# Kernel optimization log

Hardware: AMD Instinct MI355X
Metric: run time of the kernel (lower is better)

Reference implementation:

```python
import jax, jax.numpy as jnp
import numpy as np

EMBED_DIM = 1024
NUM_HEADS = 16
HEAD_DIM = EMBED_DIM // NUM_HEADS


def setup_inputs() -> dict:
    key = jax.random.key(0)
    ks = jax.random.split(key, 5)
    x = jax.random.normal(ks[0], (2, 2048, EMBED_DIM), dtype=jnp.float32)
    s_in = 1.0 / np.sqrt(EMBED_DIM)
    W_qkv = jax.random.uniform(ks[1], (EMBED_DIM, 3 * EMBED_DIM), minval=-s_in, maxval=s_in, dtype=jnp.float32)
    b_qkv = jax.random.uniform(ks[2], (3 * EMBED_DIM,), minval=-s_in, maxval=s_in, dtype=jnp.float32)
    W_out = jax.random.uniform(ks[3], (EMBED_DIM, EMBED_DIM), minval=-s_in, maxval=s_in, dtype=jnp.float32)
    b_out = jax.random.uniform(ks[4], (EMBED_DIM,), minval=-s_in, maxval=s_in, dtype=jnp.float32)
    return {"x": x, "W_qkv": W_qkv, "b_qkv": b_qkv, "W_out": W_out, "b_out": b_out}


def reference(x, W_qkv, b_qkv, W_out, b_out):
    B, S, D = x.shape
    H, Dh = NUM_HEADS, HEAD_DIM
    qkv = x @ W_qkv + b_qkv                       # [B, S, 3D]
    q, k, v = jnp.split(qkv, 3, axis=-1)
    # [B, S, D] -> [B, H, S, Dh]
    q = q.reshape(B, S, H, Dh).transpose(0, 2, 1, 3)
    k = k.reshape(B, S, H, Dh).transpose(0, 2, 1, 3)
    v = v.reshape(B, S, H, Dh).transpose(0, 2, 1, 3)
    scores = jnp.einsum('bhqd,bhkd->bhqk', q, k) / jnp.sqrt(jnp.float32(Dh))
    probs = jax.nn.softmax(scores, axis=-1)       # [B, H, S, S]
    attn = jnp.einsum('bhqk,bhkd->bhqd', probs, v)
    attn = attn.transpose(0, 2, 1, 3).reshape(B, S, D)
    return attn @ W_out + b_out
```

## Files before the change

### kernel.cpp

```cpp
#include <hip/hip_runtime.h>
#include <hip/hip_bf16.h>

#define DEV __device__ __forceinline__

typedef __bf16 bf16x8 __attribute__((ext_vector_type(8)));
typedef float f32x4 __attribute__((ext_vector_type(4)));
typedef float f32x16 __attribute__((ext_vector_type(16)));
using u16 = unsigned short;
using u32 = unsigned int;

static constexpr int S = 2048;
static constexpr int D = 1024;
static constexpr float SCQ = 0.125f * 1.44269504088896340736f;

DEV u16 f2bf(float f) {
  unsigned u = __builtin_bit_cast(unsigned, f);
  u += 0x7fffu + ((u >> 16) & 1u);
  return (u16)(u >> 16);
}
DEV u16 f2bfr(float f) {
  return (u16)((__builtin_bit_cast(u32, f) + 0x8000u) >> 16);
}
DEV u32 pk2(float a, float b) {
  u32 ua = __builtin_bit_cast(u32, a) + 0x8000u;
  u32 ub = __builtin_bit_cast(u32, b) + 0x8000u;
  return __builtin_amdgcn_perm(ub, ua, 0x07060302);
}

__global__ __launch_bounds__(256) void k_prep(const float* __restrict__ x, u16* __restrict__ Xb,
                                              const float* __restrict__ Wqkv, u16* __restrict__ WqkvT,
                                              const float* __restrict__ Wout, u16* __restrict__ WoutT) {
  __shared__ float t[32][33];
  const int bid = blockIdx.x;
  const int tid = threadIdx.x;
  if (bid < 4096) {
    const int i = bid * 256 + tid;
    const float4 v = reinterpret_cast<const float4*>(x)[i];
    ushort4 o;
    o.x = f2bf(v.x); o.y = f2bf(v.y); o.z = f2bf(v.z); o.w = f2bf(v.w);
    reinterpret_cast<ushort4*>(Xb)[i] = o;
    return;
  }
  const float* in;
  u16* out;
  int R, C, bx, by;
  if (bid < 4096 + 3072) {
    const int b = bid - 4096;
    in = Wqkv; out = WqkvT; R = 1024; C = 3072;
    bx = b % 96; by = b / 96;
  } else {
    const int b = bid - 7168;
    in = Wout; out = WoutT; R = 1024; C = 1024;
    bx = b & 31; by = b >> 5;
  }
  const int tx = tid & 31, ty = tid >> 5;
  const int c0 = bx * 32, r0 = by * 32;
  for (int i = ty; i < 32; i += 8)
    t[i][tx] = in[(size_t)(r0 + i) * C + c0 + tx];
  __syncthreads();
  for (int i = ty; i < 32; i += 8)
    out[(size_t)(c0 + i) * R + r0 + tx] = f2bf(t[tx][i]);
}

template <int MODE, int TN>
__global__ __launch_bounds__(256) void k_gemm(const u16* __restrict__ A, const u16* __restrict__ Bt,
                                              const float* __restrict__ bias, int M, int N, int K,
                                              u16* __restrict__ Qb, u16* __restrict__ Kb,
                                              u16* __restrict__ Vt, float* __restrict__ outF) {
  constexpr int NJ = TN / 32;
  __shared__ u16 As[128][40];
  __shared__ u16 Bs[TN][40];
  const int tid = threadIdx.x;
  const int lane = tid & 63, wave = tid >> 6;
  const int l15 = lane & 15, quad = lane >> 4;
  const int m0 = blockIdx.y * 128, n0 = blockIdx.x * TN;
  const int wm = (wave >> 1) * 64, wn = (wave & 1) * (TN / 2);
  const int row0 = tid >> 2, c0 = (tid & 3) * 8;
  const int row1 = row0 + 64;

  f32x4 acc[4][NJ];
#pragma unroll
  for (int i = 0; i < 4; i++)
#pragma unroll
    for (int j = 0; j < NJ; j++) acc[i][j] = (f32x4){0.f, 0.f, 0.f, 0.f};

  uint4 pa0 = *reinterpret_cast<const uint4*>(&A[(size_t)(m0 + row0) * K + c0]);
  uint4 pa1 = *reinterpret_cast<const uint4*>(&A[(size_t)(m0 + row1) * K + c0]);
  uint4 pb0 = *reinterpret_cast<const uint4*>(&Bt[(size_t)(n0 + row0) * K + c0]);
  uint4 pb1;
  if constexpr (TN == 128) pb1 = *reinterpret_cast<const uint4*>(&Bt[(size_t)(n0 + row1) * K + c0]);

  for (int kk = 0; kk < K; kk += 32) {
    __syncthreads();
    *reinterpret_cast<uint4*>(&As[row0][c0]) = pa0;
    *reinterpret_cast<uint4*>(&As[row1][c0]) = pa1;
    *reinterpret_cast<uint4*>(&Bs[row0 & (TN - 1)][c0]) = pb0;
    if constexpr (TN == 128) *reinterpret_cast<uint4*>(&Bs[row1][c0]) = pb1;
    __syncthreads();
    if (kk + 32 < K) {
      pa0 = *reinterpret_cast<const uint4*>(&A[(size_t)(m0 + row0) * K + kk + 32 + c0]);
      pa1 = *reinterpret_cast<const uint4*>(&A[(size_t)(m0 + row1) * K + kk + 32 + c0]);
      pb0 = *reinterpret_cast<const uint4*>(&Bt[(size_t)(n0 + row0) * K + kk + 32 + c0]);
      if constexpr (TN == 128)
        pb1 = *reinterpret_cast<const uint4*>(&Bt[(size_t)(n0 + row1) * K + kk + 32 + c0]);
    }
    bf16x8 af[4], bfv[NJ];
#pragma unroll
    for (int i = 0; i < 4; i++)
      af[i] = *reinterpret_cast<const bf16x8*>(&As[wm + i * 16 + l15][quad * 8]);
#pragma unroll
    for (int j = 0; j < NJ; j++)
      bfv[j] = *reinterpret_cast<const bf16x8*>(&Bs[wn + j * 16 + l15][quad * 8]);
#pragma unroll
    for (int i = 0; i < 4; i++)
#pragma unroll
      for (int j = 0; j < NJ; j++)
        acc[i][j] = __builtin_amdgcn_mfma_f32_16x16x32_bf16(af[i], bfv[j], acc[i][j], 0, 0, 0);
  }

  if constexpr (MODE == 0) {
    __shared__ u16 LT[64][136];
    if (n0 >= 2048) {
      const int b = m0 >> 11, sbase = m0 & 2047;
#pragma unroll
      for (int p = 0; p < 2; p++) {
        __syncthreads();
        if ((wave & 1) == p) {
#pragma unroll
          for (int j = 0; j < NJ; j++) {
            const int n = n0 + wn + j * 16 + l15;
            const float vb = bias[n];
#pragma unroll
            for (int i = 0; i < 4; i++) {
              uint2 pw;
              pw.x = pk2(acc[i][j][0] + vb, acc[i][j][1] + vb);
              pw.y = pk2(acc[i][j][2] + vb, acc[i][j][3] + vb);
              *reinterpret_cast<uint2*>(&LT[j * 16 + l15][wm + i * 16 + quad * 4]) = pw;
            }
          }
        }
        __syncthreads();
        const int h = ((n0 - 2048) >> 6) + p;
        const int bh = b * 16 + h;
        const int nl = tid >> 2, cc = (tid & 3) * 32;
        u16* dst = &Vt[((size_t)bh * 64 + nl) * S + sbase + cc];
#pragma unroll
        for (int k = 0; k < 4; k++)
          reinterpret_cast<uint4*>(dst)[k] = *reinterpret_cast<const uint4*>(&LT[nl][cc + k * 8]);
      }
    } else {
#pragma unroll
      for (int i = 0; i < 4; i++) {
#pragma unroll
        for (int j = 0; j < NJ; j++) {
#pragma unroll
          for (int r = 0; r < 4; r++) {
            const int m = m0 + wm + i * 16 + quad * 4 + r;
            const int n = n0 + wn + j * 16 + l15;
            const float v = acc[i][j][r] + bias[n];
            const int h = (n >> 6) & 15, dh = n & 63;
            const int b = m >> 11, s = m & 2047;
            const int bh = b * 16 + h;
            if (n < 1024) Qb[((size_t)bh * S + s) * 64 + dh] = f2bfr(v * SCQ);
            else          Kb[((size_t)bh * S + s) * 64 + dh] = f2bfr(v);
          }
        }
      }
    }
  } else {
#pragma unroll
    for (int i = 0; i < 4; i++)
#pragma unroll
      for (int j = 0; j < NJ; j++)
#pragma unroll
        for (int r = 0; r < 4; r++) {
          const int m = m0 + wm + i * 16 + quad * 4 + r;
          const int n = n0 + wn + j * 16 + l15;
          outF[(size_t)m * N + n] = acc[i][j][r] + bias[n];
        }
  }
}

__global__ __launch_bounds__(256, 2) void k_attn(const u16* __restrict__ Qb,
                                                 const u16* __restrict__ Kb,
                                                 const u16* __restrict__ Vt,
                                                 u16* __restrict__ attnB) {
  __shared__ u16 Ks[64][72];
  __shared__ u16 Vs[64][72];
  __shared__ u16 Pl[4][32][72];
  const int bh = blockIdx.y;
  const int q0 = blockIdx.x * 128;
  const int tid = threadIdx.x;
  const int lane = tid & 63, wave = tid >> 6;
  const int l31 = lane & 31, hi = lane >> 5;
  const u16* Qh = Qb + (size_t)bh * S * 64;
  const u16* Kh = Kb + (size_t)bh * S * 64;
  const u16* Vh = Vt + (size_t)bh * 64 * S;
  const int qrow = q0 + wave * 32 + l31;
  bf16x8 qf[4];
#pragma unroll
  for (int f = 0; f < 4; f++)
    qf[f] = *reinterpret_cast<const bf16x8*>(&Qh[(size_t)qrow * 64 + f * 16 + hi * 8]);

  const int r0 = tid >> 3, c0 = (tid & 7) * 8;

  float li = 0.f;
  f32x16 o0, o1;
#pragma unroll
  for (int r = 0; r < 16; r++) { o0[r] = 0.f; o1[r] = 0.f; }

  uint4 pk0 = *reinterpret_cast<const uint4*>(&Kh[(size_t)r0 * 64 + c0]);
  uint4 pk1 = *reinterpret_cast<const uint4*>(&Kh[(size_t)(r0 + 32) * 64 + c0]);
  uint4 pv0 = *reinterpret_cast<const uint4*>(&Vh[(size_t)r0 * S + c0]);
  uint4 pv1 = *reinterpret_cast<const uint4*>(&Vh[(size_t)(r0 + 32) * S + c0]);

  for (int kb = 0; kb < S / 64; kb++) {
    __syncthreads();
    *reinterpret_cast<uint4*>(&Ks[r0][c0]) = pk0;
    *reinterpret_cast<uint4*>(&Ks[r0 + 32][c0]) = pk1;
    *reinterpret_cast<uint4*>(&Vs[r0][c0]) = pv0;
    *reinterpret_cast<uint4*>(&Vs[r0 + 32][c0]) = pv1;
    __syncthreads();
    if (kb + 1 < S / 64) {
      const u16* Kn = Kh + (size_t)(kb + 1) * 64 * 64;
      pk0 = *reinterpret_cast<const uint4*>(&Kn[(size_t)r0 * 64 + c0]);
      pk1 = *reinterpret_cast<const uint4*>(&Kn[(size_t)(r0 + 32) * 64 + c0]);
      pv0 = *reinterpret_cast<const uint4*>(&Vh[(size_t)r0 * S + (kb + 1) * 64 + c0]);
      pv1 = *reinterpret_cast<const uint4*>(&Vh[(size_t)(r0 + 32) * S + (kb + 1) * 64 + c0]);
    }
    f32x16 z[2];
#pragma unroll
    for (int kt = 0; kt < 2; kt++) {
#pragma unroll
      for (int r = 0; r < 16; r++) z[kt][r] = 0.f;
#pragma unroll
      for (int f = 0; f < 4; f++) {
        const bf16x8 a = *reinterpret_cast<const bf16x8*>(&Ks[kt * 32 + l31][f * 16 + hi * 8]);
        z[kt] = __builtin_amdgcn_mfma_f32_32x32x16_bf16(a, qf[f], z[kt], 0, 0, 0);
      }
    }
    float s0 = 0.f, s1 = 0.f, s2 = 0.f, s3 = 0.f;
#pragma unroll
    for (int kt = 0; kt < 2; kt++)
#pragma unroll
      for (int r = 0; r < 16; r++) {
        const float p = __builtin_amdgcn_exp2f(z[kt][r]);
        z[kt][r] = p;
        if ((r & 3) == 0) s0 += p; else if ((r & 3) == 1) s1 += p;
        else if ((r & 3) == 2) s2 += p; else s3 += p;
      }
    li += (s0 + s1) + (s2 + s3);
#pragma unroll
    for (int kt = 0; kt < 2; kt++)
#pragma unroll
      for (int g = 0; g < 4; g++) {
        uint2 pw;
        pw.x = pk2(z[kt][g * 4 + 0], z[kt][g * 4 + 1]);
        pw.y = pk2(z[kt][g * 4 + 2], z[kt][g * 4 + 3]);
        *reinterpret_cast<uint2*>(&Pl[wave][l31][kt * 32 + g * 8 + hi * 4]) = pw;
      }
#pragma unroll
    for (int f = 0; f < 4; f++) {
      const bf16x8 bp = *reinterpret_cast<const bf16x8*>(&Pl[wave][l31][f * 16 + hi * 8]);
      const bf16x8 av0 = *reinterpret_cast<const bf16x8*>(&Vs[l31][f * 16 + hi * 8]);
      const bf16x8 av1 = *reinterpret_cast<const bf16x8*>(&Vs[32 + l31][f * 16 + hi * 8]);
      o0 = __builtin_amdgcn_mfma_f32_32x32x16_bf16(av0, bp, o0, 0, 0, 0);
      o1 = __builtin_amdgcn_mfma_f32_32x32x16_bf16(av1, bp, o1, 0, 0, 0);
    }
  }
  li += __shfl_xor(li, 32);
  const float inv = 1.f / li;
#pragma unroll
  for (int dt = 0; dt < 2; dt++) {
    const f32x16& od = dt ? o1 : o0;
#pragma unroll
    for (int g = 0; g < 4; g++) {
      uint2 ow;
      ow.x = pk2(od[g * 4 + 0] * inv, od[g * 4 + 1] * inv);
      ow.y = pk2(od[g * 4 + 2] * inv, od[g * 4 + 3] * inv);
      *reinterpret_cast<uint2*>(&Pl[wave][l31][dt * 32 + g * 8 + hi * 4]) = ow;
    }
  }
  const int b = bh >> 4, h = bh & 15;
  const int mbase = b * S + q0 + wave * 32;
  const int qr = lane >> 1, ch = (lane & 1) * 32;
  u16* dst = &attnB[(size_t)(mbase + qr) * D + h * 64 + ch];
#pragma unroll
  for (int c = 0; c < 4; c++)
    reinterpret_cast<uint4*>(dst)[c] = *reinterpret_cast<const uint4*>(&Pl[wave][qr][ch + c * 8]);
}

extern "C" void kernel_launch(void* const* d_in, const int* in_sizes, int n_in,
                              void* d_out, int out_size, void* d_ws, size_t ws_size,
                              hipStream_t stream) {
  const float* x = (const float*)d_in[0];
  const float* Wqkv = (const float*)d_in[1];
  const float* bqkv = (const float*)d_in[2];
  const float* Wout = (const float*)d_in[3];
  const float* bout = (const float*)d_in[4];
  float* out = (float*)d_out;

  char* p = (char*)d_ws;
  u16* Xb = (u16*)p;    p += (size_t)4096 * 1024 * 2;
  u16* WqkvT = (u16*)p; p += (size_t)3072 * 1024 * 2;
  u16* WoutT = (u16*)p; p += (size_t)1024 * 1024 * 2;
  u16* Qb = (u16*)p;    p += (size_t)32 * 2048 * 64 * 2;
  u16* Kb = (u16*)p;    p += (size_t)32 * 2048 * 64 * 2;
  u16* Vt = (u16*)p;    p += (size_t)32 * 64 * 2048 * 2;
  u16* attnB = (u16*)p; p += (size_t)4096 * 1024 * 2;

  k_prep<<<4096 + 3072 + 1024, 256, 0, stream>>>(x, Xb, Wqkv, WqkvT, Wout, WoutT);
  k_gemm<0, 128><<<dim3(3072 / 128, 4096 / 128), 256, 0, stream>>>(
      Xb, WqkvT, bqkv, 4096, 3072, 1024, Qb, Kb, Vt, nullptr);
  k_attn<<<dim3(2048 / 128, 32), 256, 0, stream>>>(Qb, Kb, Vt, attnB);
  k_gemm<1, 64><<<dim3(1024 / 64, 4096 / 128), 256, 0, stream>>>(
      attnB, WoutT, bout, 4096, 1024, 1024, nullptr, nullptr, nullptr, out);
}
```

Before: 200.6 us.

## Split attention over two key halves and merge partials in a combine kernel

```diff
diff --git a/kernel.cpp b/kernel.cpp
--- a/kernel.cpp
+++ b/kernel.cpp
@@ -181,14 +181,16 @@
   }
 }
 
-__global__ __launch_bounds__(256, 2) void k_attn(const u16* __restrict__ Qb,
+__global__ __launch_bounds__(256, 4) void k_attn(const u16* __restrict__ Qb,
                                                  const u16* __restrict__ Kb,
                                                  const u16* __restrict__ Vt,
-                                                 u16* __restrict__ attnB) {
+                                                 u16* __restrict__ Op0, u16* __restrict__ Op1,
+                                                 float* __restrict__ Li) {
   __shared__ u16 Ks[64][72];
   __shared__ u16 Vs[64][72];
   __shared__ u16 Pl[4][32][72];
-  const int bh = blockIdx.y;
+  const int bh = blockIdx.z;
+  const int ks = blockIdx.y;
   const int q0 = blockIdx.x * 128;
   const int tid = threadIdx.x;
   const int lane = tid & 63, wave = tid >> 6;
@@ -203,25 +205,26 @@
     qf[f] = *reinterpret_cast<const bf16x8*>(&Qh[(size_t)qrow * 64 + f * 16 + hi * 8]);
 
   const int r0 = tid >> 3, c0 = (tid & 7) * 8;
+  const int kb0 = ks * 16, kb1 = kb0 + 16;
 
   float li = 0.f;
   f32x16 o0, o1;
 #pragma unroll
   for (int r = 0; r < 16; r++) { o0[r] = 0.f; o1[r] = 0.f; }
 
-  uint4 pk0 = *reinterpret_cast<const uint4*>(&Kh[(size_t)r0 * 64 + c0]);
-  uint4 pk1 = *reinterpret_cast<const uint4*>(&Kh[(size_t)(r0 + 32) * 64 + c0]);
-  uint4 pv0 = *reinterpret_cast<const uint4*>(&Vh[(size_t)r0 * S + c0]);
-  uint4 pv1 = *reinterpret_cast<const uint4*>(&Vh[(size_t)(r0 + 32) * S + c0]);
-
-  for (int kb = 0; kb < S / 64; kb++) {
+  uint4 pk0 = *reinterpret_cast<const uint4*>(&Kh[(size_t)(kb0 * 64 + r0) * 64 + c0]);
+  uint4 pk1 = *reinterpret_cast<const uint4*>(&Kh[(size_t)(kb0 * 64 + r0 + 32) * 64 + c0]);
+  uint4 pv0 = *reinterpret_cast<const uint4*>(&Vh[(size_t)r0 * S + kb0 * 64 + c0]);
+  uint4 pv1 = *reinterpret_cast<const uint4*>(&Vh[(size_t)(r0 + 32) * S + kb0 * 64 + c0]);
+
+  for (int kb = kb0; kb < kb1; kb++) {
     __syncthreads();
     *reinterpret_cast<uint4*>(&Ks[r0][c0]) = pk0;
     *reinterpret_cast<uint4*>(&Ks[r0 + 32][c0]) = pk1;
     *reinterpret_cast<uint4*>(&Vs[r0][c0]) = pv0;
     *reinterpret_cast<uint4*>(&Vs[r0 + 32][c0]) = pv1;
     __syncthreads();
-    if (kb + 1 < S / 64) {
+    if (kb + 1 < kb1) {
       const u16* Kn = Kh + (size_t)(kb + 1) * 64 * 64;
       pk0 = *reinterpret_cast<const uint4*>(&Kn[(size_t)r0 * 64 + c0]);
       pk1 = *reinterpret_cast<const uint4*>(&Kn[(size_t)(r0 + 32) * 64 + c0]);
@@ -269,25 +272,50 @@
     }
   }
   li += __shfl_xor(li, 32);
-  const float inv = 1.f / li;
+  if (hi == 0) Li[((size_t)ks * 32 + bh) * 2048 + qrow] = li;
 #pragma unroll
   for (int dt = 0; dt < 2; dt++) {
     const f32x16& od = dt ? o1 : o0;
 #pragma unroll
     for (int g = 0; g < 4; g++) {
       uint2 ow;
-      ow.x = pk2(od[g * 4 + 0] * inv, od[g * 4 + 1] * inv);
-      ow.y = pk2(od[g * 4 + 2] * inv, od[g * 4 + 3] * inv);
+      ow.x = pk2(od[g * 4 + 0], od[g * 4 + 1]);
+      ow.y = pk2(od[g * 4 + 2], od[g * 4 + 3]);
       *reinterpret_cast<uint2*>(&Pl[wave][l31][dt * 32 + g * 8 + hi * 4]) = ow;
     }
   }
   const int b = bh >> 4, h = bh & 15;
   const int mbase = b * S + q0 + wave * 32;
   const int qr = lane >> 1, ch = (lane & 1) * 32;
-  u16* dst = &attnB[(size_t)(mbase + qr) * D + h * 64 + ch];
+  u16* Opx = ks ? Op1 : Op0;
+  u16* dst = &Opx[(size_t)(mbase + qr) * D + h * 64 + ch];
 #pragma unroll
   for (int c = 0; c < 4; c++)
     reinterpret_cast<uint4*>(dst)[c] = *reinterpret_cast<const uint4*>(&Pl[wave][qr][ch + c * 8]);
+}
+
+__global__ __launch_bounds__(256) void k_combine(const u16* __restrict__ Op0,
+                                                 const u16* __restrict__ Op1,
+                                                 const float* __restrict__ Li,
+                                                 u16* __restrict__ attnB) {
+  const int i = blockIdx.x * 256 + threadIdx.x;
+  const int e = i * 4;
+  const int m = e >> 10, n = e & 1023;
+  const int b = m >> 11, s = m & 2047, h = n >> 6;
+  const int li_idx = ((b << 4) + h) * 2048 + s;
+  const float inv = 1.f / (Li[li_idx] + Li[65536 + li_idx]);
+  const uint2 a = reinterpret_cast<const uint2*>(Op0)[i];
+  const uint2 c = reinterpret_cast<const uint2*>(Op1)[i];
+  const float v0 = __builtin_bit_cast(float, a.x << 16) + __builtin_bit_cast(float, c.x << 16);
+  const float v1 = __builtin_bit_cast(float, a.x & 0xffff0000u) +
+                   __builtin_bit_cast(float, c.x & 0xffff0000u);
+  const float v2 = __builtin_bit_cast(float, a.y << 16) + __builtin_bit_cast(float, c.y << 16);
+  const float v3 = __builtin_bit_cast(float, a.y & 0xffff0000u) +
+                   __builtin_bit_cast(float, c.y & 0xffff0000u);
+  uint2 o;
+  o.x = pk2(v0 * inv, v1 * inv);
+  o.y = pk2(v2 * inv, v3 * inv);
+  reinterpret_cast<uint2*>(attnB)[i] = o;
 }
 
 extern "C" void kernel_launch(void* const* d_in, const int* in_sizes, int n_in,
@@ -308,11 +336,15 @@
   u16* Kb = (u16*)p;    p += (size_t)32 * 2048 * 64 * 2;
   u16* Vt = (u16*)p;    p += (size_t)32 * 64 * 2048 * 2;
   u16* attnB = (u16*)p; p += (size_t)4096 * 1024 * 2;
+  u16* Op1 = (u16*)p;   p += (size_t)4096 * 1024 * 2;
+  float* Li = (float*)p; p += (size_t)2 * 32 * 2048 * 4;
+  u16* Op0 = Xb;
 
   k_prep<<<4096 + 3072 + 1024, 256, 0, stream>>>(x, Xb, Wqkv, WqkvT, Wout, WoutT);
   k_gemm<0, 128><<<dim3(3072 / 128, 4096 / 128), 256, 0, stream>>>(
       Xb, WqkvT, bqkv, 4096, 3072, 1024, Qb, Kb, Vt, nullptr);
-  k_attn<<<dim3(2048 / 128, 32), 256, 0, stream>>>(Qb, Kb, Vt, attnB);
+  k_attn<<<dim3(16, 2, 32), 256, 0, stream>>>(Qb, Kb, Vt, Op0, Op1, Li);
+  k_combine<<<4096, 256, 0, stream>>>(Op0, Op1, Li, attnB);
   k_gemm<1, 64><<<dim3(1024 / 64, 4096 / 128), 256, 0, stream>>>(
       attnB, WoutT, bout, 4096, 1024, 1024, nullptr, nullptr, nullptr, out);
 }
```

Result: slower. 205.3 us (+2.3%).

## Double GEMM K-tile to 64, alias epilogue LDS buffer, add occupancy hint

Applied to the files above, without the earlier changes.

```diff
diff --git a/kernel.cpp b/kernel.cpp
--- a/kernel.cpp
+++ b/kernel.cpp
@@ -63,20 +63,22 @@
 }
 
 template <int MODE, int TN>
-__global__ __launch_bounds__(256) void k_gemm(const u16* __restrict__ A, const u16* __restrict__ Bt,
-                                              const float* __restrict__ bias, int M, int N, int K,
-                                              u16* __restrict__ Qb, u16* __restrict__ Kb,
-                                              u16* __restrict__ Vt, float* __restrict__ outF) {
+__global__ __launch_bounds__(256, 3) void k_gemm(const u16* __restrict__ A, const u16* __restrict__ Bt,
+                                                 const float* __restrict__ bias, int M, int N, int K,
+                                                 u16* __restrict__ Qb, u16* __restrict__ Kb,
+                                                 u16* __restrict__ Vt, float* __restrict__ outF) {
   constexpr int NJ = TN / 32;
-  __shared__ u16 As[128][40];
-  __shared__ u16 Bs[TN][40];
+  constexpr int NB = (TN == 128) ? 4 : 2;
+  __shared__ u16 As[128][72];
+  __shared__ u16 Bs[TN][72];
   const int tid = threadIdx.x;
   const int lane = tid & 63, wave = tid >> 6;
   const int l15 = lane & 15, quad = lane >> 4;
   const int m0 = blockIdx.y * 128, n0 = blockIdx.x * TN;
   const int wm = (wave >> 1) * 64, wn = (wave & 1) * (TN / 2);
-  const int row0 = tid >> 2, c0 = (tid & 3) * 8;
-  const int row1 = row0 + 64;
+  const int arow = tid >> 1, acol = (tid & 1) * 32;
+  const int brow = (TN == 128) ? (tid >> 1) : (tid >> 2);
+  const int bcol = (TN == 128) ? ((tid & 1) * 32) : ((tid & 3) * 16);
 
   f32x4 acc[4][NJ];
 #pragma unroll
@@ -84,42 +86,50 @@
 #pragma unroll
     for (int j = 0; j < NJ; j++) acc[i][j] = (f32x4){0.f, 0.f, 0.f, 0.f};
 
-  uint4 pa0 = *reinterpret_cast<const uint4*>(&A[(size_t)(m0 + row0) * K + c0]);
-  uint4 pa1 = *reinterpret_cast<const uint4*>(&A[(size_t)(m0 + row1) * K + c0]);
-  uint4 pb0 = *reinterpret_cast<const uint4*>(&Bt[(size_t)(n0 + row0) * K + c0]);
-  uint4 pb1;
-  if constexpr (TN == 128) pb1 = *reinterpret_cast<const uint4*>(&Bt[(size_t)(n0 + row1) * K + c0]);
-
-  for (int kk = 0; kk < K; kk += 32) {
+  uint4 pa[4], pb[NB];
+#pragma unroll
+  for (int u = 0; u < 4; u++)
+    pa[u] = *reinterpret_cast<const uint4*>(&A[(size_t)(m0 + arow) * K + acol + u * 8]);
+#pragma unroll
+  for (int u = 0; u < NB; u++)
+    pb[u] = *reinterpret_cast<const uint4*>(&Bt[(size_t)(n0 + brow) * K + bcol + u * 8]);
+
+  for (int kk = 0; kk < K; kk += 64) {
     __syncthreads();
-    *reinterpret_cast<uint4*>(&As[row0][c0]) = pa0;
-    *reinterpret_cast<uint4*>(&As[row1][c0]) = pa1;
-    *reinterpret_cast<uint4*>(&Bs[row0 & (TN - 1)][c0]) = pb0;
-    if constexpr (TN == 128) *reinterpret_cast<uint4*>(&Bs[row1][c0]) = pb1;
+#pragma unroll
+    for (int u = 0; u < 4; u++)
+      *reinterpret_cast<uint4*>(&As[arow][acol + u * 8]) = pa[u];
+#pragma unroll
+    for (int u = 0; u < NB; u++)
+      *reinterpret_cast<uint4*>(&Bs[brow][bcol + u * 8]) = pb[u];
     __syncthreads();
-    if (kk + 32 < K) {
-      pa0 = *reinterpret_cast<const uint4*>(&A[(size_t)(m0 + row0) * K + kk + 32 + c0]);
-      pa1 = *reinterpret_cast<const uint4*>(&A[(size_t)(m0 + row1) * K + kk + 32 + c0]);
-      pb0 = *reinterpret_cast<const uint4*>(&Bt[(size_t)(n0 + row0) * K + kk + 32 + c0]);
-      if constexpr (TN == 128)
-        pb1 = *reinterpret_cast<const uint4*>(&Bt[(size_t)(n0 + row1) * K + kk + 32 + c0]);
-    }
-    bf16x8 af[4], bfv[NJ];
-#pragma unroll
-    for (int i = 0; i < 4; i++)
-      af[i] = *reinterpret_cast<const bf16x8*>(&As[wm + i * 16 + l15][quad * 8]);
-#pragma unroll
-    for (int j = 0; j < NJ; j++)
-      bfv[j] = *reinterpret_cast<const bf16x8*>(&Bs[wn + j * 16 + l15][quad * 8]);
-#pragma unroll
-    for (int i = 0; i < 4; i++)
+    if (kk + 64 < K) {
+#pragma unroll
+      for (int u = 0; u < 4; u++)
+        pa[u] = *reinterpret_cast<const uint4*>(&A[(size_t)(m0 + arow) * K + kk + 64 + acol + u * 8]);
+#pragma unroll
+      for (int u = 0; u < NB; u++)
+        pb[u] = *reinterpret_cast<const uint4*>(&Bt[(size_t)(n0 + brow) * K + kk + 64 + bcol + u * 8]);
+    }
+#pragma unroll
+    for (int h = 0; h < 2; h++) {
+      bf16x8 af[4], bfv[NJ];
+#pragma unroll
+      for (int i = 0; i < 4; i++)
+        af[i] = *reinterpret_cast<const bf16x8*>(&As[wm + i * 16 + l15][h * 32 + quad * 8]);
 #pragma unroll
       for (int j = 0; j < NJ; j++)
-        acc[i][j] = __builtin_amdgcn_mfma_f32_16x16x32_bf16(af[i], bfv[j], acc[i][j], 0, 0, 0);
+        bfv[j] = *reinterpret_cast<const bf16x8*>(&Bs[wn + j * 16 + l15][h * 32 + quad * 8]);
+#pragma unroll
+      for (int i = 0; i < 4; i++)
+#pragma unroll
+        for (int j = 0; j < NJ; j++)
+          acc[i][j] = __builtin_amdgcn_mfma_f32_16x16x32_bf16(af[i], bfv[j], acc[i][j], 0, 0, 0);
+    }
   }
 
   if constexpr (MODE == 0) {
-    __shared__ u16 LT[64][136];
+    u16(*LT)[136] = reinterpret_cast<u16(*)[136]>(&As[0][0]);
     if (n0 >= 2048) {
       const int b = m0 >> 11, sbase = m0 & 2047;
 #pragma unroll
```

Measured after the change: 311.2 us. 1.55x slower.

## Fuse x bf16 conversion into QKV GEMM and halve attention block size

Applied to the files above, without the earlier changes.

```diff
diff --git a/kernel.cpp b/kernel.cpp
--- a/kernel.cpp
+++ b/kernel.cpp
@@ -27,29 +27,19 @@
   return __builtin_amdgcn_perm(ub, ua, 0x07060302);
 }
 
-__global__ __launch_bounds__(256) void k_prep(const float* __restrict__ x, u16* __restrict__ Xb,
-                                              const float* __restrict__ Wqkv, u16* __restrict__ WqkvT,
+__global__ __launch_bounds__(256) void k_prep(const float* __restrict__ Wqkv, u16* __restrict__ WqkvT,
                                               const float* __restrict__ Wout, u16* __restrict__ WoutT) {
   __shared__ float t[32][33];
   const int bid = blockIdx.x;
   const int tid = threadIdx.x;
-  if (bid < 4096) {
-    const int i = bid * 256 + tid;
-    const float4 v = reinterpret_cast<const float4*>(x)[i];
-    ushort4 o;
-    o.x = f2bf(v.x); o.y = f2bf(v.y); o.z = f2bf(v.z); o.w = f2bf(v.w);
-    reinterpret_cast<ushort4*>(Xb)[i] = o;
-    return;
-  }
   const float* in;
   u16* out;
   int R, C, bx, by;
-  if (bid < 4096 + 3072) {
-    const int b = bid - 4096;
+  if (bid < 3072) {
     in = Wqkv; out = WqkvT; R = 1024; C = 3072;
-    bx = b % 96; by = b / 96;
+    bx = bid % 96; by = bid / 96;
   } else {
-    const int b = bid - 7168;
+    const int b = bid - 3072;
     in = Wout; out = WoutT; R = 1024; C = 1024;
     bx = b & 31; by = b >> 5;
   }
@@ -63,7 +53,7 @@
 }
 
 template <int MODE, int TN>
-__global__ __launch_bounds__(256) void k_gemm(const u16* __restrict__ A, const u16* __restrict__ Bt,
+__global__ __launch_bounds__(256) void k_gemm(const void* __restrict__ Ap, const u16* __restrict__ Bt,
                                               const float* __restrict__ bias, int M, int N, int K,
                                               u16* __restrict__ Qb, u16* __restrict__ Kb,
                                               u16* __restrict__ Vt, float* __restrict__ outF) {
@@ -77,6 +67,8 @@
   const int wm = (wave >> 1) * 64, wn = (wave & 1) * (TN / 2);
   const int row0 = tid >> 2, c0 = (tid & 3) * 8;
   const int row1 = row0 + 64;
+  const float* Af = (const float*)Ap;
+  const u16* Ab = (const u16*)Ap;
 
   f32x4 acc[4][NJ];
 #pragma unroll
@@ -84,22 +76,48 @@
 #pragma unroll
     for (int j = 0; j < NJ; j++) acc[i][j] = (f32x4){0.f, 0.f, 0.f, 0.f};
 
-  uint4 pa0 = *reinterpret_cast<const uint4*>(&A[(size_t)(m0 + row0) * K + c0]);
-  uint4 pa1 = *reinterpret_cast<const uint4*>(&A[(size_t)(m0 + row1) * K + c0]);
-  uint4 pb0 = *reinterpret_cast<const uint4*>(&Bt[(size_t)(n0 + row0) * K + c0]);
-  uint4 pb1;
+  float4 qa0, qa1, qa2, qa3;
+  uint4 pa0, pa1;
+  uint4 pb0, pb1;
+  if constexpr (MODE == 0) {
+    qa0 = *reinterpret_cast<const float4*>(&Af[(size_t)(m0 + row0) * K + c0]);
+    qa1 = *reinterpret_cast<const float4*>(&Af[(size_t)(m0 + row0) * K + c0 + 4]);
+    qa2 = *reinterpret_cast<const float4*>(&Af[(size_t)(m0 + row1) * K + c0]);
+    qa3 = *reinterpret_cast<const float4*>(&Af[(size_t)(m0 + row1) * K + c0 + 4]);
+  } else {
+    pa0 = *reinterpret_cast<const uint4*>(&Ab[(size_t)(m0 + row0) * K + c0]);
+    pa1 = *reinterpret_cast<const uint4*>(&Ab[(size_t)(m0 + row1) * K + c0]);
+  }
+  pb0 = *reinterpret_cast<const uint4*>(&Bt[(size_t)(n0 + row0) * K + c0]);
   if constexpr (TN == 128) pb1 = *reinterpret_cast<const uint4*>(&Bt[(size_t)(n0 + row1) * K + c0]);
 
   for (int kk = 0; kk < K; kk += 32) {
     __syncthreads();
-    *reinterpret_cast<uint4*>(&As[row0][c0]) = pa0;
-    *reinterpret_cast<uint4*>(&As[row1][c0]) = pa1;
+    if constexpr (MODE == 0) {
+      uint4 wa0, wa1;
+      wa0.x = pk2(qa0.x, qa0.y); wa0.y = pk2(qa0.z, qa0.w);
+      wa0.z = pk2(qa1.x, qa1.y); wa0.w = pk2(qa1.z, qa1.w);
+      wa1.x = pk2(qa2.x, qa2.y); wa1.y = pk2(qa2.z, qa2.w);
+      wa1.z = pk2(qa3.x, qa3.y); wa1.w = pk2(qa3.z, qa3.w);
+      *reinterpret_cast<uint4*>(&As[row0][c0]) = wa0;
+      *reinterpret_cast<uint4*>(&As[row1][c0]) = wa1;
+    } else {
+      *reinterpret_cast<uint4*>(&As[row0][c0]) = pa0;
+      *reinterpret_cast<uint4*>(&As[row1][c0]) = pa1;
+    }
     *reinterpret_cast<uint4*>(&Bs[row0 & (TN - 1)][c0]) = pb0;
     if constexpr (TN == 128) *reinterpret_cast<uint4*>(&Bs[row1][c0]) = pb1;
     __syncthreads();
     if (kk + 32 < K) {
-      pa0 = *reinterpret_cast<const uint4*>(&A[(size_t)(m0 + row0) * K + kk + 32 + c0]);
-      pa1 = *reinterpret_cast<const uint4*>(&A[(size_t)(m0 + row1) * K + kk + 32 + c0]);
+      if constexpr (MODE == 0) {
+        qa0 = *reinterpret_cast<const float4*>(&Af[(size_t)(m0 + row0) * K + kk + 32 + c0]);
+        qa1 = *reinterpret_cast<const float4*>(&Af[(size_t)(m0 + row0) * K + kk + 32 + c0 + 4]);
+        qa2 = *reinterpret_cast<const float4*>(&Af[(size_t)(m0 + row1) * K + kk + 32 + c0]);
+        qa3 = *reinterpret_cast<const float4*>(&Af[(size_t)(m0 + row1) * K + kk + 32 + c0 + 4]);
+      } else {
+        pa0 = *reinterpret_cast<const uint4*>(&Ab[(size_t)(m0 + row0) * K + kk + 32 + c0]);
+        pa1 = *reinterpret_cast<const uint4*>(&Ab[(size_t)(m0 + row1) * K + kk + 32 + c0]);
+      }
       pb0 = *reinterpret_cast<const uint4*>(&Bt[(size_t)(n0 + row0) * K + kk + 32 + c0]);
       if constexpr (TN == 128)
         pb1 = *reinterpret_cast<const uint4*>(&Bt[(size_t)(n0 + row1) * K + kk + 32 + c0]);
@@ -181,15 +199,15 @@
   }
 }
 
-__global__ __launch_bounds__(256, 2) void k_attn(const u16* __restrict__ Qb,
-                                                 const u16* __restrict__ Kb,
-                                                 const u16* __restrict__ Vt,
-                                                 u16* __restrict__ attnB) {
+__global__ __launch_bounds__(128) void k_attn(const u16* __restrict__ Qb,
+                                              const u16* __restrict__ Kb,
+                                              const u16* __restrict__ Vt,
+                                              u16* __restrict__ attnB) {
   __shared__ u16 Ks[64][72];
   __shared__ u16 Vs[64][72];
-  __shared__ u16 Pl[4][32][72];
+  __shared__ u16 Pl[2][32][72];
   const int bh = blockIdx.y;
-  const int q0 = blockIdx.x * 128;
+  const int q0 = blockIdx.x * 64;
   const int tid = threadIdx.x;
   const int lane = tid & 63, wave = tid >> 6;
   const int l31 = lane & 31, hi = lane >> 5;
@@ -209,24 +227,28 @@
 #pragma unroll
   for (int r = 0; r < 16; r++) { o0[r] = 0.f; o1[r] = 0.f; }
 
-  uint4 pk0 = *reinterpret_cast<const uint4*>(&Kh[(size_t)r0 * 64 + c0]);
-  uint4 pk1 = *reinterpret_cast<const uint4*>(&Kh[(size_t)(r0 + 32) * 64 + c0]);
-  uint4 pv0 = *reinterpret_cast<const uint4*>(&Vh[(size_t)r0 * S + c0]);
-  uint4 pv1 = *reinterpret_cast<const uint4*>(&Vh[(size_t)(r0 + 32) * S + c0]);
+  uint4 pk[4], pv[4];
+#pragma unroll
+  for (int u = 0; u < 4; u++) {
+    pk[u] = *reinterpret_cast<const uint4*>(&Kh[(size_t)(r0 + 16 * u) * 64 + c0]);
+    pv[u] = *reinterpret_cast<const uint4*>(&Vh[(size_t)(r0 + 16 * u) * S + c0]);
+  }
 
   for (int kb = 0; kb < S / 64; kb++) {
     __syncthreads();
-    *reinterpret_cast<uint4*>(&Ks[r0][c0]) = pk0;
-    *reinterpret_cast<uint4*>(&Ks[r0 + 32][c0]) = pk1;
-    *reinterpret_cast<uint4*>(&Vs[r0][c0]) = pv0;
-    *reinterpret_cast<uint4*>(&Vs[r0 + 32][c0]) = pv1;
+#pragma unroll
+    for (int u = 0; u < 4; u++) {
+      *reinterpret_cast<uint4*>(&Ks[r0 + 16 * u][c0]) = pk[u];
+      *reinterpret_cast<uint4*>(&Vs[r0 + 16 * u][c0]) = pv[u];
+    }
     __syncthreads();
     if (kb + 1 < S / 64) {
       const u16* Kn = Kh + (size_t)(kb + 1) * 64 * 64;
-      pk0 = *reinterpret_cast<const uint4*>(&Kn[(size_t)r0 * 64 + c0]);
-      pk1 = *reinterpret_cast<const uint4*>(&Kn[(size_t)(r0 + 32) * 64 + c0]);
-      pv0 = *reinterpret_cast<const uint4*>(&Vh[(size_t)r0 * S + (kb + 1) * 64 + c0]);
-      pv1 = *reinterpret_cast<const uint4*>(&Vh[(size_t)(r0 + 32) * S + (kb + 1) * 64 + c0]);
+#pragma unroll
+      for (int u = 0; u < 4; u++) {
+        pk[u] = *reinterpret_cast<const uint4*>(&Kn[(size_t)(r0 + 16 * u) * 64 + c0]);
+        pv[u] = *reinterpret_cast<const uint4*>(&Vh[(size_t)(r0 + 16 * u) * S + (kb + 1) * 64 + c0]);
+      }
     }
     f32x16 z[2];
 #pragma unroll
@@ -301,7 +323,6 @@
   float* out = (float*)d_out;
 
   char* p = (char*)d_ws;
-  u16* Xb = (u16*)p;    p += (size_t)4096 * 1024 * 2;
   u16* WqkvT = (u16*)p; p += (size_t)3072 * 1024 * 2;
   u16* WoutT = (u16*)p; p += (size_t)1024 * 1024 * 2;
   u16* Qb = (u16*)p;    p += (size_t)32 * 2048 * 64 * 2;
@@ -309,10 +330,10 @@
   u16* Vt = (u16*)p;    p += (size_t)32 * 64 * 2048 * 2;
   u16* attnB = (u16*)p; p += (size_t)4096 * 1024 * 2;
 
-  k_prep<<<4096 + 3072 + 1024, 256, 0, stream>>>(x, Xb, Wqkv, WqkvT, Wout, WoutT);
+  k_prep<<<3072 + 1024, 256, 0, stream>>>(Wqkv, WqkvT, Wout, WoutT);
   k_gemm<0, 128><<<dim3(3072 / 128, 4096 / 128), 256, 0, stream>>>(
-      Xb, WqkvT, bqkv, 4096, 3072, 1024, Qb, Kb, Vt, nullptr);
-  k_attn<<<dim3(2048 / 128, 32), 256, 0, stream>>>(Qb, Kb, Vt, attnB);
+      (const void*)x, WqkvT, bqkv, 4096, 3072, 1024, Qb, Kb, Vt, nullptr);
+  k_attn<<<dim3(2048 / 64, 32), 128, 0, stream>>>(Qb, Kb, Vt, attnB);
   k_gemm<1, 64><<<dim3(1024 / 64, 4096 / 128), 256, 0, stream>>>(
-      attnB, WoutT, bout, 4096, 1024, 1024, nullptr, nullptr, nullptr, out);
-}
+      (const void*)attnB, WoutT, bout, 4096, 1024, 1024, nullptr, nullptr, nullptr, out);
+}
```

Measured after the change: 308.1 us. +53.6%, slower.
